# Optimization experiments

Measured on AMD Instinct MI355X. Metric: run time of the kernel, lower is better.

The kernel has to match this reference:

```python
import jax, jax.numpy as jnp
import numpy as np
from jax import lax

SEQ, BATCH, FEAT = 64, 32768, 15
H1 = H2 = H3 = 4  # hidden sizes from the source module


def setup_inputs() -> dict:
    key = jax.random.key(0)
    ks = jax.random.split(key, 11)
    s = 0.1
    return {
        "x": jax.random.normal(ks[0], (SEQ, BATCH, FEAT), jnp.float32),
        "w1": jax.random.normal(ks[1], (H1, FEAT), jnp.float32) * s,
        "b1": jax.random.normal(ks[2], (H1,), jnp.float32) * s,
        "w2": jax.random.normal(ks[3], (H2, H1), jnp.float32) * s,
        "b2": jax.random.normal(ks[4], (H2,), jnp.float32) * s,
        "w_ih": jax.random.normal(ks[5], (4 * H3, H2), jnp.float32) * s,
        "w_hh": jax.random.normal(ks[6], (4 * H3, H3), jnp.float32) * s,
        "b_ih": jax.random.normal(ks[7], (4 * H3,), jnp.float32) * s,
        "b_hh": jax.random.normal(ks[8], (4 * H3,), jnp.float32) * s,
        "w3": jax.random.normal(ks[9], (1, H3), jnp.float32) * s,
        "b3": jax.random.normal(ks[10], (1,), jnp.float32) * s,
    }


def reference(x, w1, b1, w2, b2, w_ih, w_hh, b_ih, b_hh, w3, b3):
    seq, batch, _ = x.shape
    hidden = w_hh.shape[1]
    # front-end MLP: fc1 -> relu -> fc2 -> sigmoid   (applied per timestep)
    h1 = jax.nn.relu(jnp.einsum('sbf,hf->sbh', x, w1) + b1)          # [S,B,H1]
    h2 = jax.nn.sigmoid(jnp.einsum('sbh,gh->sbg', h1, w2) + b2)      # [S,B,H2]
    # precompute input-to-gate projections for all timesteps: [S,B,4H]
    gx = jnp.einsum('sbh,gh->sbg', h2, w_ih) + b_ih + b_hh

    def step(carry, gxt):
        h, c = carry
        gates = gxt + h @ w_hh.T                                      # [B,4H]
        i, f, g, o = jnp.split(gates, 4, axis=-1)                     # torch order i,f,g,o
        i = jax.nn.sigmoid(i)
        f = jax.nn.sigmoid(f)
        g = jnp.tanh(g)
        o = jax.nn.sigmoid(o)
        c = f * c + i * g
        h = o * jnp.tanh(c)
        return (h, c), None

    h0 = jnp.zeros((batch, hidden), x.dtype)
    c0 = jnp.zeros((batch, hidden), x.dtype)
    (h_last, _), _ = lax.scan(step, (h0, c0), gx)                     # last-step hidden [B,H3]
    out = jax.nn.sigmoid(h_last @ w3.T + b3)                          # [B,1]
    return out.reshape(batch)
```

## Files before the change

### kernel.cpp

```cpp
#include <hip/hip_runtime.h>

#define SEQ   64
#define BATCH 32768
#define FEAT  15
#define SLAB  (BATCH * FEAT)

#define LOG2E 1.4426950408889634f

typedef float v2f __attribute__((ext_vector_type(2)));

__device__ __forceinline__ float fast_rcp(float x) { return __builtin_amdgcn_rcpf(x); }
__device__ __forceinline__ float ex2(float x)      { return __builtin_amdgcn_exp2f(x); }
__device__ __forceinline__ float sig2(float t)     { return fast_rcp(1.0f + ex2(t)); }

template <int CTRL>
__device__ __forceinline__ float qmov(float v) {
    return __int_as_float(
        __builtin_amdgcn_mov_dpp(__float_as_int(v), CTRL, 0xf, 0xf, false));
}

__device__ __forceinline__ v2f fma2(v2f a, v2f b, v2f c) { return a * b + c; }

struct Fq { float a, b, c, d; };

__global__ __launch_bounds__(256, 2) void lstm_fused(
    const float* __restrict__ x,
    const float* __restrict__ w1,  const float* __restrict__ b1,
    const float* __restrict__ w2,  const float* __restrict__ b2,
    const float* __restrict__ wih, const float* __restrict__ whh,
    const float* __restrict__ bih, const float* __restrict__ bhh,
    const float* __restrict__ w3,  const float* __restrict__ b3,
    float* __restrict__ out)
{
    const int tid = threadIdx.x;
    const int w   = tid >> 6;
    const int l   = tid & 63;
    const int u   = l & 3;
    const int e   = l >> 2;
    const int elem = blockIdx.x * 64 + w * 16 + e;

    const int qoff = (u == 3) ? 11 : 4 * u;
    const float* xp = x + (size_t)elem * FEAT + qoff;

    v2f W1a[4], W1b[4], SE[4];
#pragma unroll
    for (int j = 0; j < 4; ++j) {
        const float* r = w1 + j * FEAT + qoff;
        W1a[j] = v2f{(u == 3) ? 0.0f : r[0], r[1]};
        W1b[j] = v2f{r[2], r[3]};
        SE[j]  = v2f{(u == 0) ? b1[j] : 0.0f, 0.0f};
    }
    float W2s[4];
#pragma unroll
    for (int j = 0; j < 4; ++j) W2s[j] = -LOG2E * w2[u * 4 + j];
    const float B2v = -LOG2E * b2[u];
    v2f WIp[4][2], WHp[4][2], BIg[4];
#pragma unroll
    for (int g = 0; g < 4; ++g) {
        const float sg = (g == 2) ? (2.0f * LOG2E) : -LOG2E;
        const int row = (g * 4 + u) * 4;
        WIp[g][0] = v2f{sg * wih[row + 0], sg * wih[row + 1]};
        WIp[g][1] = v2f{sg * wih[row + 2], sg * wih[row + 3]};
        WHp[g][0] = v2f{sg * whh[row + 0], sg * whh[row + 1]};
        WHp[g][1] = v2f{sg * whh[row + 2], sg * whh[row + 3]};
        BIg[g]    = v2f{sg * (bih[g * 4 + u] + bhh[g * 4 + u]), 0.0f};
    }
    const float W3v = -LOG2E * w3[u];
    const float B3v = -LOG2E * b3[0];

    float h = 0.0f, c = 0.0f;

    auto step = [&](Fq q) {
        const v2f f01 = v2f{q.a, q.b}, f23 = v2f{q.c, q.d};
        float P[4];
#pragma unroll
        for (int j = 0; j < 4; ++j) {
            const v2f p2 = fma2(W1a[j], f01, fma2(W1b[j], f23, SE[j]));
            P[j] = p2.x + p2.y;
        }
#pragma unroll
        for (int j = 0; j < 4; ++j) {
            P[j] += qmov<0xB1>(P[j]);
            P[j] += qmov<0x4E>(P[j]);
            P[j] = fmaxf(P[j], 0.0f);
        }
        const float a2n = fmaf(W2s[0], P[0], fmaf(W2s[1], P[1],
                          fmaf(W2s[2], P[2], fmaf(W2s[3], P[3], B2v))));
        const float h2 = sig2(a2n);
        const v2f q01 = v2f{qmov<0x00>(h2), qmov<0x55>(h2)};
        const v2f q23 = v2f{qmov<0xAA>(h2), qmov<0xFF>(h2)};
        v2f A[4];
#pragma unroll
        for (int g = 0; g < 4; ++g)
            A[g] = fma2(WIp[g][0], q01, fma2(WIp[g][1], q23, BIg[g]));
        const v2f h01 = v2f{qmov<0x00>(h), qmov<0x55>(h)};
        const v2f h23 = v2f{qmov<0xAA>(h), qmov<0xFF>(h)};
#pragma unroll
        for (int g = 0; g < 4; ++g)
            A[g] = fma2(WHp[g][0], h01, fma2(WHp[g][1], h23, A[g]));
        const float ig = sig2(A[0].x + A[0].y);
        const float fg = sig2(A[1].x + A[1].y);
        const float gt = fmaf(-2.0f, sig2(A[2].x + A[2].y), 1.0f);
        const float og = sig2(A[3].x + A[3].y);
        c = fmaf(fg, c, ig * gt);
        const float tc = fmaf(-2.0f, sig2(c * (2.0f * LOG2E)), 1.0f);
        h = og * tc;
    };

    Fq Qa[8], Qb[8];
    auto ld4 = [](const float* p) {
        Fq r; r.a = p[0]; r.b = p[1]; r.c = p[2]; r.d = p[3]; return r;
    };
    auto prefetch8 = [&](Fq* Q, const float* base) {
#pragma unroll
        for (int j = 0; j < 8; ++j) Q[j] = ld4(base + (size_t)j * SLAB);
    };
    auto compute8 = [&](Fq* Q) {
#pragma unroll
        for (int j = 0; j < 8; ++j) step(Q[j]);
    };

    prefetch8(Qa, xp);
#pragma unroll 1
    for (int i = 0; i < 3; ++i) {
        const float* bft = xp + (size_t)(16 * i + 8) * SLAB;
        prefetch8(Qb, bft);
        __builtin_amdgcn_sched_barrier(0);
        compute8(Qa);
        prefetch8(Qa, bft + (size_t)8 * SLAB);
        __builtin_amdgcn_sched_barrier(0);
        compute8(Qb);
    }
    prefetch8(Qb, xp + (size_t)56 * SLAB);
    __builtin_amdgcn_sched_barrier(0);
    compute8(Qa);
    compute8(Qb);

    float p = W3v * h;
    p += qmov<0xB1>(p);
    p += qmov<0x4E>(p);
    if (u == 0) out[elem] = sig2(p + B3v);
}

extern "C" void kernel_launch(void* const* d_in, const int* in_sizes, int n_in,
                              void* d_out, int out_size, void* d_ws, size_t ws_size,
                              hipStream_t stream) {
    (void)in_sizes; (void)n_in; (void)d_ws; (void)ws_size; (void)out_size;
    const float* x   = (const float*)d_in[0];
    const float* w1  = (const float*)d_in[1];
    const float* b1  = (const float*)d_in[2];
    const float* w2  = (const float*)d_in[3];
    const float* b2  = (const float*)d_in[4];
    const float* wih = (const float*)d_in[5];
    const float* whh = (const float*)d_in[6];
    const float* bih = (const float*)d_in[7];
    const float* bhh = (const float*)d_in[8];
    const float* w3  = (const float*)d_in[9];
    const float* b3  = (const float*)d_in[10];
    float* out = (float*)d_out;

    lstm_fused<<<dim3(512), dim3(256), 0, stream>>>(
        x, w1, b1, w2, b2, wih, whh, bih, bhh, w3, b3, out);
}
```

Measured before the change: 33.50 us.

## Stream x through LDS with direct global_load_lds and an 8-deep ring buffer

Each wave now issues 16-byte global_load_lds transfers that move its contiguous 16-element x row slab for a timestep straight into a per-wave LDS ring of 8 buffers. It then reads four rotated float4s per lane from LDS so that every lane holds full feature vectors. Lane u now computes hidden unit u of fc1 over all 15 features, which removes the two-stage DPP reduction, and manual vmcnt/lgkmcnt waits keep 7 timesteps of loads in flight. The aim is fully coalesced 16-byte loads, fewer VGPRs for register prefetch, and a simpler fc1, in exchange for LDS round trips and hand-tuned wait counts that depend on exact instruction ordering.

After: 30.31 us. -9.5%, faster.

```diff
diff --git a/kernel.cpp b/kernel.cpp
--- a/kernel.cpp
+++ b/kernel.cpp
@@ -3,11 +3,12 @@
 #define SEQ   64
 #define BATCH 32768
 #define FEAT  15
-#define SLAB  (BATCH * FEAT)
+#define SLABBYTES (BATCH * FEAT * 4)
 
 #define LOG2E 1.4426950408889634f
 
 typedef float v2f __attribute__((ext_vector_type(2)));
+typedef float v4f __attribute__((ext_vector_type(4)));
 
 __device__ __forceinline__ float fast_rcp(float x) { return __builtin_amdgcn_rcpf(x); }
 __device__ __forceinline__ float ex2(float x)      { return __builtin_amdgcn_exp2f(x); }
@@ -21,7 +22,17 @@
 
 __device__ __forceinline__ v2f fma2(v2f a, v2f b, v2f c) { return a * b + c; }
 
-struct Fq { float a, b, c, d; };
+template <int N>
+__device__ __forceinline__ void waitv() {
+    asm volatile("s_waitcnt vmcnt(%0)" :: "n"(N) : "memory");
+}
+template <int N>
+__device__ __forceinline__ void waitlg() {
+    asm volatile("s_waitcnt lgkmcnt(%0)" :: "n"(N) : "memory");
+}
+
+typedef const __attribute__((address_space(1))) void gas_t;
+typedef __attribute__((address_space(3))) void las_t;
 
 __global__ __launch_bounds__(256, 2) void lstm_fused(
     const float* __restrict__ x,
@@ -32,24 +43,43 @@
     const float* __restrict__ w3,  const float* __restrict__ b3,
     float* __restrict__ out)
 {
+    __shared__ __align__(16) float lds[4][8][256];
+
     const int tid = threadIdx.x;
     const int w   = tid >> 6;
     const int l   = tid & 63;
     const int u   = l & 3;
     const int e   = l >> 2;
-    const int elem = blockIdx.x * 64 + w * 16 + e;
+    const int ebase = blockIdx.x * 64 + w * 16;
+    const int elem  = ebase + e;
 
-    const int qoff = (u == 3) ? 11 : 4 * u;
-    const float* xp = x + (size_t)elem * FEAT + qoff;
+    const int perm_e = (e + (e >> 2)) & 3;
+    const int p      = (u - perm_e) & 3;
+    const int inrow  = (p < 3) ? p * 16 : 44;
+    uint32_t off = (uint32_t)(ebase + e) * 60u + (uint32_t)inrow;
 
-    v2f W1a[4], W1b[4], SE[4];
+    auto gload = [&](int b, uint32_t o) {
+        __builtin_amdgcn_global_load_lds(
+            (gas_t*)((const char*)x + o),
+            (las_t*)&lds[w][b][0], 16, 0, 0);
+    };
+
+    int sb[4];
 #pragma unroll
-    for (int j = 0; j < 4; ++j) {
-        const float* r = w1 + j * FEAT + qoff;
-        W1a[j] = v2f{(u == 3) ? 0.0f : r[0], r[1]};
-        W1b[j] = v2f{r[2], r[3]};
-        SE[j]  = v2f{(u == 0) ? b1[j] : 0.0f, 0.0f};
-    }
+    for (int pp = 0; pp < 4; ++pp) sb[pp] = (4 * e + ((pp + perm_e) & 3)) * 4;
+
+    auto ldrow = [&](int b, v4f& F0, v4f& F1, v4f& F2, v4f& F3) {
+        const float* B = &lds[w][b][0];
+        F0 = *(const v4f*)(B + sb[0]);
+        F1 = *(const v4f*)(B + sb[1]);
+        F2 = *(const v4f*)(B + sb[2]);
+        F3 = *(const v4f*)(B + sb[3]);
+    };
+
+    float W1[FEAT];
+#pragma unroll
+    for (int f = 0; f < FEAT; ++f) W1[f] = w1[u * FEAT + f];
+    const float B1v = b1[u];
     float W2s[4];
 #pragma unroll
     for (int j = 0; j < 4; ++j) W2s[j] = -LOG2E * w2[u * 4 + j];
@@ -70,22 +100,22 @@
 
     float h = 0.0f, c = 0.0f;
 
-    auto step = [&](Fq q) {
-        const v2f f01 = v2f{q.a, q.b}, f23 = v2f{q.c, q.d};
-        float P[4];
-#pragma unroll
-        for (int j = 0; j < 4; ++j) {
-            const v2f p2 = fma2(W1a[j], f01, fma2(W1b[j], f23, SE[j]));
-            P[j] = p2.x + p2.y;
-        }
-#pragma unroll
-        for (int j = 0; j < 4; ++j) {
-            P[j] += qmov<0xB1>(P[j]);
-            P[j] += qmov<0x4E>(P[j]);
-            P[j] = fmaxf(P[j], 0.0f);
-        }
-        const float a2n = fmaf(W2s[0], P[0], fmaf(W2s[1], P[1],
-                          fmaf(W2s[2], P[2], fmaf(W2s[3], P[3], B2v))));
+    auto step = [&](v4f F0, v4f F1, v4f F2, v4f F3) {
+        float a0 = B1v, a1 = 0.0f, a2 = 0.0f;
+        a0 = fmaf(W1[0], F0.x, a0);  a0 = fmaf(W1[1], F0.y, a0);
+        a0 = fmaf(W1[2], F0.z, a0);  a0 = fmaf(W1[3], F0.w, a0);
+        a0 = fmaf(W1[4], F1.x, a0);
+        a1 = fmaf(W1[5], F1.y, a1);  a1 = fmaf(W1[6], F1.z, a1);
+        a1 = fmaf(W1[7], F1.w, a1);  a1 = fmaf(W1[8], F2.x, a1);
+        a1 = fmaf(W1[9], F2.y, a1);
+        a2 = fmaf(W1[10], F2.z, a2); a2 = fmaf(W1[11], F2.w, a2);
+        a2 = fmaf(W1[12], F3.y, a2); a2 = fmaf(W1[13], F3.z, a2);
+        a2 = fmaf(W1[14], F3.w, a2);
+        const float h1 = fmaxf(a0 + (a1 + a2), 0.0f);
+        const float t0 = qmov<0x00>(h1), t1 = qmov<0x55>(h1);
+        const float t2 = qmov<0xAA>(h1), t3 = qmov<0xFF>(h1);
+        const float a2n = fmaf(W2s[0], t0, fmaf(W2s[1], t1,
+                          fmaf(W2s[2], t2, fmaf(W2s[3], t3, B2v))));
         const float h2 = sig2(a2n);
         const v2f q01 = v2f{qmov<0x00>(h2), qmov<0x55>(h2)};
         const v2f q23 = v2f{qmov<0xAA>(h2), qmov<0xFF>(h2)};
@@ -107,39 +137,43 @@
         h = og * tc;
     };
 
-    Fq Qa[8], Qb[8];
-    auto ld4 = [](const float* p) {
-        Fq r; r.a = p[0]; r.b = p[1]; r.c = p[2]; r.d = p[3]; return r;
-    };
-    auto prefetch8 = [&](Fq* Q, const float* base) {
 #pragma unroll
-        for (int j = 0; j < 8; ++j) Q[j] = ld4(base + (size_t)j * SLAB);
-    };
-    auto compute8 = [&](Fq* Q) {
+    for (int b = 0; b < 8; ++b) { gload(b, off); off += SLABBYTES; }
+    waitv<7>();
+    __builtin_amdgcn_sched_barrier(0);
+    v4f F0, F1, F2, F3;
+    ldrow(0, F0, F1, F2, F3);
+
+#pragma unroll 1
+    for (int ph = 0; ph < 7; ++ph) {
 #pragma unroll
-        for (int j = 0; j < 8; ++j) step(Q[j]);
-    };
+        for (int j = 0; j < 8; ++j) {
+            waitv<6>();
+            __builtin_amdgcn_sched_barrier(0);
+            v4f G0, G1, G2, G3;
+            ldrow((j + 1) & 7, G0, G1, G2, G3);
+            waitlg<4>();
+            __builtin_amdgcn_sched_barrier(0);
+            gload(j, off);  off += SLABBYTES;
+            step(F0, F1, F2, F3);
+            F0 = G0; F1 = G1; F2 = G2; F3 = G3;
+        }
+    }
+#define EPI(JJ, NN)                                                   \
+    {   waitv<NN>();                                                  \
+        __builtin_amdgcn_sched_barrier(0);                            \
+        v4f G0, G1, G2, G3;                                           \
+        ldrow(((JJ) + 1) & 7, G0, G1, G2, G3);                        \
+        step(F0, F1, F2, F3);                                         \
+        F0 = G0; F1 = G1; F2 = G2; F3 = G3; }
+    EPI(0, 6) EPI(1, 5) EPI(2, 4) EPI(3, 3) EPI(4, 2) EPI(5, 1) EPI(6, 0)
+#undef EPI
+    step(F0, F1, F2, F3);
 
-    prefetch8(Qa, xp);
-#pragma unroll 1
-    for (int i = 0; i < 3; ++i) {
-        const float* bft = xp + (size_t)(16 * i + 8) * SLAB;
-        prefetch8(Qb, bft);
-        __builtin_amdgcn_sched_barrier(0);
-        compute8(Qa);
-        prefetch8(Qa, bft + (size_t)8 * SLAB);
-        __builtin_amdgcn_sched_barrier(0);
-        compute8(Qb);
-    }
-    prefetch8(Qb, xp + (size_t)56 * SLAB);
-    __builtin_amdgcn_sched_barrier(0);
-    compute8(Qa);
-    compute8(Qb);
-
-    float p = W3v * h;
-    p += qmov<0xB1>(p);
-    p += qmov<0x4E>(p);
-    if (u == 0) out[elem] = sig2(p + B3v);
+    float pr = W3v * h;
+    pr += qmov<0xB1>(pr);
+    pr += qmov<0x4E>(pr);
+    if (u == 0) out[elem] = sig2(pr + B3v);
 }
 
 extern "C" void kernel_launch(void* const* d_in, const int* in_sizes, int n_in,
```
